# Performance work log

Hardware: AMD Instinct MI355X
Metric: run time of the kernel (lower is better)

The kernel has to match this reference:

```python
import jax, jax.numpy as jnp
import numpy as np

B, L, C = 16, 450, 768
MID = 256
K = 8912
TEMP = 0.07
ENT_TEMP = 0.01
EPS_NORM = 1e-12


def _l2norm(v):
    n = jnp.sqrt(jnp.sum(v * v, axis=-1, keepdims=True))
    return v / jnp.maximum(n, EPS_NORM)


def setup_inputs() -> dict:
    key = jax.random.key(0)
    k1, k2, k3, k4 = jax.random.split(key, 4)
    x = jax.random.normal(k1, (B, L, C), dtype=jnp.float32)
    W_down = jax.random.normal(k2, (C, MID), dtype=jnp.float32) * (1.0 / np.sqrt(C))
    b_down = jnp.zeros((MID,), dtype=jnp.float32)
    bound = 1.0 / np.sqrt(MID)
    embedding = jax.random.uniform(k3, (K, MID), dtype=jnp.float32, minval=-bound, maxval=bound)
    return {"x": x, "W_down": W_down, "b_down": b_down, "embedding": embedding}


def reference(x, W_down, b_down, embedding):
    Bx, Lx, Cx = x.shape
    # down projection: [B,L,C] -> [B,L,MID]
    z = jnp.einsum('blc,cm->blm', x, W_down) + b_down
    zf = z.reshape(Bx * Lx, MID)
    zn = _l2norm(zf)                       # [N, MID]
    en = _l2norm(embedding)                # [K, MID]
    # squared euclidean distance on the unit sphere: ||a-b||^2 = 2 - 2 a.b
    d = 2.0 - 2.0 * jnp.einsum('nm,km->nk', zn, en)   # [N, K]
    idx = jnp.argmin(d, axis=1)            # [N]
    # codebook usage (no-grad stats)
    occ = jnp.bincount(idx, length=K)
    code_book_usage = jnp.mean((occ > 0).astype(jnp.float32))
    # soft assignment probs (hard_quant branch)
    logits = -d / TEMP
    probs = jax.nn.softmax(logits, axis=1)
    z_q = en[idx]                          # [N, MID]
    vq_loss = jnp.mean((z_q - jax.lax.stop_gradient(zn)) ** 2)
    commit_loss = jnp.mean((jax.lax.stop_gradient(z_q) - zn) ** 2)
    # straight-through estimator
    z_q_ste = zn + jax.lax.stop_gradient(z_q - zn)
    # entropy loss on affinity = -d at entropy temperature
    fa = -d / ENT_TEMP
    p = jax.nn.softmax(fa, axis=-1)
    lp = jax.nn.log_softmax(fa, axis=-1)
    avg_probs = jnp.mean(p, axis=0)
    avg_entropy = -jnp.sum(avg_probs * jnp.log(avg_probs + 1e-5))
    sample_entropy = -jnp.mean(jnp.sum(p * lp, axis=-1))
    entropy_loss = sample_entropy - avg_entropy
    return (z_q_ste.reshape(Bx, Lx, MID), probs.reshape(Bx, Lx, K),
            code_book_usage, vq_loss, commit_loss, entropy_loss)
```

## Files before the change

### kernel.cpp

```cpp
#include <hip/hip_runtime.h>
#include <stdint.h>

#define N_TOK 7200
#define N_PAD 7232
#define K_CODE 8912
#define K_PAD 8960
#define N_KT 140
#define MID 256
#define C_DIM 768
#define INV_TEMP (1.0f/0.07f)
#define INV_ETEMP 100.0f
#define MARGIN 0.02f
#define CAND_CAP 64
#define EPS_N 1e-12f

typedef __attribute__((ext_vector_type(8))) short short8;
typedef __attribute__((ext_vector_type(4))) float f32x4;

__device__ __forceinline__ unsigned short f2bf(float f) {
    unsigned u = __float_as_uint(f);
    u += 0x7fffu + ((u >> 16) & 1u);
    return (unsigned short)(u >> 16);
}
__device__ __forceinline__ float bf2f(unsigned short h) {
    return __uint_as_float(((unsigned)h) << 16);
}

__global__ void k_init(float* ap_acc, int* used, float* acc4, int* ccnt) {
    int i = blockIdx.x * 256 + threadIdx.x;
    if (i < K_CODE) { ap_acc[i] = 0.f; used[i] = 0; }
    if (i < N_TOK) ccnt[i] = 0;
    if (i < 4) acc4[i] = 0.f;
}

__global__ void k_wsplit(const float* __restrict__ W,
                         unsigned short* __restrict__ wt_h,
                         unsigned short* __restrict__ wt_l) {
    int i = blockIdx.x * 256 + threadIdx.x;
    if (i >= C_DIM * MID) return;
    int c = i / MID, t = i % MID;
    float v = W[i];
    unsigned short h = f2bf(v);
    unsigned short l = f2bf(v - bf2f(h));
    wt_h[t * C_DIM + c] = h;
    wt_l[t * C_DIM + c] = l;
}

__global__ void k_ennorm(const float* __restrict__ emb,
                         float* __restrict__ en,
                         unsigned short* __restrict__ en_h) {
    int n = blockIdx.x, t = threadIdx.x;
    float v = emb[n * MID + t];
    __shared__ float sb[256];
    sb[t] = v * v; __syncthreads();
    for (int s = 128; s > 0; s >>= 1) { if (t < s) sb[t] += sb[t + s]; __syncthreads(); }
    float nn = sqrtf(sb[0]);
    float o = v / fmaxf(nn, EPS_N);
    en[n * MID + t] = o;
    en_h[n * MID + t] = f2bf(o);
}

__global__ __launch_bounds__(256) void k_zgemm(const float* __restrict__ x,
                                               const unsigned short* __restrict__ wt_h,
                                               const unsigned short* __restrict__ wt_l,
                                               float* __restrict__ zbuf) {
    __shared__ unsigned short ls[4 * 64 * 72];
    unsigned short* xh = ls;
    unsigned short* xl = ls + 64 * 72;
    unsigned short* wh = ls + 2 * 64 * 72;
    unsigned short* wl = ls + 3 * 64 * 72;
    int tid = threadIdx.x;
    int m0 = blockIdx.y * 64;
    int t0 = blockIdx.x * 64;
    int lane = tid & 63, wv = tid >> 6;
    int quad = lane >> 4, l15 = lane & 15;
    int mrow0 = (wv >> 1) * 32, ncol0 = (wv & 1) * 32;
    f32x4 acc[2][2] = {};

    for (int ch = 0; ch < 12; ch++) {
        int c0 = ch * 64;
        for (int it = 0; it < 4; it++) {
            int r = it * 16 + (tid >> 4);
            int cq = tid & 15;
            float4 v = make_float4(0.f, 0.f, 0.f, 0.f);
            int gr = m0 + r;
            if (gr < N_TOK) v = ((const float4*)x)[(size_t)gr * (C_DIM / 4) + (c0 >> 2) + cq];
            unsigned short h0 = f2bf(v.x), h1 = f2bf(v.y), h2 = f2bf(v.z), h3 = f2bf(v.w);
            ushort4 hh = make_ushort4(h0, h1, h2, h3);
            ushort4 ll = make_ushort4(f2bf(v.x - bf2f(h0)), f2bf(v.y - bf2f(h1)),
                                      f2bf(v.z - bf2f(h2)), f2bf(v.w - bf2f(h3)));
            *((ushort4*)&xh[r * 72 + cq * 4]) = hh;
            *((ushort4*)&xl[r * 72 + cq * 4]) = ll;
        }
        for (int it = 0; it < 2; it++) {
            int r = it * 32 + (tid >> 3);
            int cq = tid & 7;
            uint4 vh = ((const uint4*)wt_h)[(size_t)(t0 + r) * (C_DIM / 8) + (c0 >> 3) + cq];
            uint4 vl = ((const uint4*)wt_l)[(size_t)(t0 + r) * (C_DIM / 8) + (c0 >> 3) + cq];
            *((uint4*)&wh[r * 72 + cq * 8]) = vh;
            *((uint4*)&wl[r * 72 + cq * 8]) = vl;
        }
        __syncthreads();
        for (int ks = 0; ks < 2; ks++) {
            int co = ks * 32 + quad * 8;
            short8 ah0 = *((const short8*)&xh[(mrow0 + l15) * 72 + co]);
            short8 ah1 = *((const short8*)&xh[(mrow0 + 16 + l15) * 72 + co]);
            short8 al0 = *((const short8*)&xl[(mrow0 + l15) * 72 + co]);
            short8 al1 = *((const short8*)&xl[(mrow0 + 16 + l15) * 72 + co]);
            short8 bh0 = *((const short8*)&wh[(ncol0 + l15) * 72 + co]);
            short8 bh1 = *((const short8*)&wh[(ncol0 + 16 + l15) * 72 + co]);
            short8 bl0 = *((const short8*)&wl[(ncol0 + l15) * 72 + co]);
            short8 bl1 = *((const short8*)&wl[(ncol0 + 16 + l15) * 72 + co]);
            acc[0][0] = __builtin_amdgcn_mfma_f32_16x16x32_bf16(ah0, bh0, acc[0][0], 0, 0, 0);
            acc[0][1] = __builtin_amdgcn_mfma_f32_16x16x32_bf16(ah0, bh1, acc[0][1], 0, 0, 0);
            acc[1][0] = __builtin_amdgcn_mfma_f32_16x16x32_bf16(ah1, bh0, acc[1][0], 0, 0, 0);
            acc[1][1] = __builtin_amdgcn_mfma_f32_16x16x32_bf16(ah1, bh1, acc[1][1], 0, 0, 0);
            acc[0][0] = __builtin_amdgcn_mfma_f32_16x16x32_bf16(ah0, bl0, acc[0][0], 0, 0, 0);
            acc[0][1] = __builtin_amdgcn_mfma_f32_16x16x32_bf16(ah0, bl1, acc[0][1], 0, 0, 0);
            acc[1][0] = __builtin_amdgcn_mfma_f32_16x16x32_bf16(ah1, bl0, acc[1][0], 0, 0, 0);
            acc[1][1] = __builtin_amdgcn_mfma_f32_16x16x32_bf16(ah1, bl1, acc[1][1], 0, 0, 0);
            acc[0][0] = __builtin_amdgcn_mfma_f32_16x16x32_bf16(al0, bh0, acc[0][0], 0, 0, 0);
            acc[0][1] = __builtin_amdgcn_mfma_f32_16x16x32_bf16(al0, bh1, acc[0][1], 0, 0, 0);
            acc[1][0] = __builtin_amdgcn_mfma_f32_16x16x32_bf16(al1, bh0, acc[1][0], 0, 0, 0);
            acc[1][1] = __builtin_amdgcn_mfma_f32_16x16x32_bf16(al1, bh1, acc[1][1], 0, 0, 0);
        }
        __syncthreads();
    }
    for (int i = 0; i < 2; i++)
        for (int j = 0; j < 2; j++)
            for (int r = 0; r < 4; r++) {
                int gr = m0 + mrow0 + i * 16 + quad * 4 + r;
                int gc = t0 + ncol0 + j * 16 + l15;
                if (gr < N_TOK) zbuf[(size_t)gr * MID + gc] = acc[i][j][r];
            }
}

__global__ void k_znorm(float* __restrict__ zbuf, const float* __restrict__ b_down,
                        unsigned short* __restrict__ zn_h) {
    int n = blockIdx.x, t = threadIdx.x;
    float v = zbuf[(size_t)n * MID + t] + b_down[t];
    __shared__ float sb[256];
    sb[t] = v * v; __syncthreads();
    for (int s = 128; s > 0; s >>= 1) { if (t < s) sb[t] += sb[t + s]; __syncthreads(); }
    float nn = sqrtf(sb[0]);
    float o = v / fmaxf(nn, EPS_N);
    zbuf[(size_t)n * MID + t] = o;
    zn_h[(size_t)n * MID + t] = f2bf(o);
}

template<int PASS>
__global__ __launch_bounds__(256) void k_dpass(const unsigned short* __restrict__ zn_h,
                                               const unsigned short* __restrict__ en_h,
                                               float4* __restrict__ part4,
                                               const float* __restrict__ rs_m,
                                               const float* __restrict__ rs_ist,
                                               const float* __restrict__ rs_is1,
                                               float* __restrict__ ap_acc,
                                               float* __restrict__ out1,
                                               int* __restrict__ ccnt,
                                               int* __restrict__ cand) {
    __shared__ __align__(16) char smem[2 * 64 * 136 * 2];
    unsigned short* at = (unsigned short*)smem;
    unsigned short* bt = at + 64 * 136;
    int tid = threadIdx.x;
    int kt = blockIdx.x, mt = blockIdx.y;
    int m0 = mt * 64, k0c = kt * 64;
    int lane = tid & 63, wv = tid >> 6;
    int quad = lane >> 4, l15 = lane & 15;
    int mrow0 = (wv >> 1) * 32, ncol0 = (wv & 1) * 32;
    f32x4 acc[2][2] = {};

    for (int ch = 0; ch < 2; ch++) {
        int c0 = ch * 128;
        for (int it = 0; it < 4; it++) {
            int r = it * 16 + (tid >> 4);
            int cq = tid & 15;
            uint4 va = ((const uint4*)zn_h)[(size_t)(m0 + r) * (MID / 8) + (c0 >> 3) + cq];
            uint4 vb = ((const uint4*)en_h)[(size_t)(k0c + r) * (MID / 8) + (c0 >> 3) + cq];
            *((uint4*)&at[r * 136 + cq * 8]) = va;
            *((uint4*)&bt[r * 136 + cq * 8]) = vb;
        }
        __syncthreads();
        for (int ks = 0; ks < 4; ks++) {
            int co = ks * 32 + quad * 8;
            short8 a0 = *((const short8*)&at[(mrow0 + l15) * 136 + co]);
            short8 a1 = *((const short8*)&at[(mrow0 + 16 + l15) * 136 + co]);
            short8 b0 = *((const short8*)&bt[(ncol0 + l15) * 136 + co]);
            short8 b1 = *((const short8*)&bt[(ncol0 + 16 + l15) * 136 + co]);
            acc[0][0] = __builtin_amdgcn_mfma_f32_16x16x32_bf16(a0, b0, acc[0][0], 0, 0, 0);
            acc[0][1] = __builtin_amdgcn_mfma_f32_16x16x32_bf16(a0, b1, acc[0][1], 0, 0, 0);
            acc[1][0] = __builtin_amdgcn_mfma_f32_16x16x32_bf16(a1, b0, acc[1][0], 0, 0, 0);
            acc[1][1] = __builtin_amdgcn_mfma_f32_16x16x32_bf16(a1, b1, acc[1][1], 0, 0, 0);
        }
        __syncthreads();
    }

    float* sd = (float*)smem;
    float* lm = sd + 64 * 68;
    float* lt = lm + 64;
    float* l1 = lt + 64;
    float* colacc = l1 + 64;

    if (PASS == 2) {
        if (tid < 64) {
            int gr = m0 + tid;
            bool okr = gr < N_TOK;
            lm[tid] = okr ? rs_m[gr] : 0.f;
            lt[tid] = okr ? rs_ist[gr] : 0.f;
            l1[tid] = okr ? rs_is1[gr] : 0.f;
        }
    }
    for (int i = 0; i < 2; i++)
        for (int j = 0; j < 2; j++)
            for (int r = 0; r < 4; r++) {
                int lr = mrow0 + i * 16 + quad * 4 + r;
                int lc = ncol0 + j * 16 + l15;
                int gc = k0c + lc;
                float dv = (gc < K_CODE) ? (2.f - 2.f * acc[i][j][r]) : 1e30f;
                sd[lr * 68 + lc] = dv;
            }
    __syncthreads();

    if (PASS == 1) {
        int rloc = wv * 16 + (lane >> 2);
        const float* rowp = sd + rloc * 68 + (lane & 3) * 16;
        float vals[16];
        float vmin = 1e30f;
        #pragma unroll
        for (int i = 0; i < 16; i++) { vals[i] = rowp[i]; vmin = fminf(vmin, vals[i]); }
        vmin = fminf(vmin, __shfl_xor(vmin, 1));
        vmin = fminf(vmin, __shfl_xor(vmin, 2));
        float st = 0.f, s1 = 0.f, s2 = 0.f;
        #pragma unroll
        for (int i = 0; i < 16; i++) {
            float dd = vmin - vals[i];
            st += __expf(dd * INV_TEMP);
            float te = dd * INV_ETEMP;
            float e = __expf(te);
            s1 += e; s2 += e * te;
        }
        st += __shfl_xor(st, 1); st += __shfl_xor(st, 2);
        s1 += __shfl_xor(s1, 1); s1 += __shfl_xor(s1, 2);
        s2 += __shfl_xor(s2, 1); s2 += __shfl_xor(s2, 2);
        if ((lane & 3) == 0) {
            int gr = m0 + rloc;
            if (gr < N_TOK) part4[(size_t)gr * N_KT + kt] = make_float4(vmin, st, s1, s2);
        }
    } else {
        int col = tid & 63, rq = tid >> 6;
        float ce = 0.f;
        #pragma unroll
        for (int r16 = 0; r16 < 16; r16++) {
            int lr = rq * 16 + r16;
            float dv = sd[lr * 68 + col];
            ce += __expf((lm[lr] - dv) * INV_ETEMP) * l1[lr];
        }
        colacc[rq * 64 + col] = ce;
        __syncthreads();
        if (tid < 64) {
            float s = colacc[tid] + colacc[64 + tid] + colacc[128 + tid] + colacc[192 + tid];
            int gc = k0c + tid;
            if (gc < K_CODE) atomicAdd(&ap_acc[gc], s);
        }
        #pragma unroll
        for (int it = 0; it < 4; it++) {
            int idx = it * 256 + tid;
            int lr = idx >> 4, c4 = idx & 15;
            int gr = m0 + lr;
            if (gr >= N_TOK) continue;
            int gc = k0c + c4 * 4;
            if (gc >= K_CODE) continue;
            float4 v = *((const float4*)(sd + lr * 68 + c4 * 4));
            float mm = lm[lr], tt = lt[lr];
            float thr = mm + MARGIN;
            if (v.x <= thr) { int p = atomicAdd(&ccnt[gr], 1); if (p < CAND_CAP) cand[gr * CAND_CAP + p] = gc + 0; }
            if (v.y <= thr) { int p = atomicAdd(&ccnt[gr], 1); if (p < CAND_CAP) cand[gr * CAND_CAP + p] = gc + 1; }
            if (v.z <= thr) { int p = atomicAdd(&ccnt[gr], 1); if (p < CAND_CAP) cand[gr * CAND_CAP + p] = gc + 2; }
            if (v.w <= thr) { int p = atomicAdd(&ccnt[gr], 1); if (p < CAND_CAP) cand[gr * CAND_CAP + p] = gc + 3; }
            float4 p;
            p.x = __expf((mm - v.x) * INV_TEMP) * tt;
            p.y = __expf((mm - v.y) * INV_TEMP) * tt;
            p.z = __expf((mm - v.z) * INV_TEMP) * tt;
            p.w = __expf((mm - v.w) * INV_TEMP) * tt;
            *((float4*)(out1 + (size_t)gr * K_CODE + gc)) = p;
        }
    }
}

__global__ void k_combine(const float4* __restrict__ part4,
                          float* __restrict__ rs_m, float* __restrict__ rs_ist,
                          float* __restrict__ rs_is1,
                          float* __restrict__ acc4) {
    int sub = threadIdx.x >> 6;
    int row = blockIdx.x * 4 + sub;
    int l = threadIdx.x & 63;
    float4 pv[3];
    float m = 1e30f;
    #pragma unroll
    for (int c = 0; c < 3; c++) {
        int t = l + c * 64;
        pv[c] = (t < N_KT) ? part4[(size_t)row * N_KT + t] : make_float4(1e30f, 0.f, 0.f, 0.f);
        m = fminf(m, pv[c].x);
    }
    #pragma unroll
    for (int s = 1; s < 64; s <<= 1) m = fminf(m, __shfl_xor(m, s));
    float st = 0.f, s1 = 0.f, s2 = 0.f;
    #pragma unroll
    for (int c = 0; c < 3; c++) {
        float mb = pv[c].x;
        int t = l + c * 64;
        if (t < N_KT && mb < 1e29f) {
            float dT = (m - mb) * INV_TEMP;
            st += __expf(dT) * pv[c].y;
            float dE = (m - mb) * INV_ETEMP;
            float e = __expf(dE);
            s1 += e * pv[c].z;
            s2 += e * (pv[c].w + dE * pv[c].z);
        }
    }
    #pragma unroll
    for (int s = 1; s < 64; s <<= 1) {
        st += __shfl_xor(st, s);
        s1 += __shfl_xor(s1, s);
        s2 += __shfl_xor(s2, s);
    }
    if (l == 0) {
        rs_m[row] = m;
        rs_ist[row] = 1.f / st;
        rs_is1[row] = 1.f / s1;
        atomicAdd(&acc4[1], s2 / s1 - __logf(s1));
    }
}

__global__ void k_refine(const float* __restrict__ zn, const float* __restrict__ en,
                         const int* __restrict__ ccnt, const int* __restrict__ cand,
                         int* __restrict__ idxb, int* __restrict__ used,
                         float* __restrict__ acc4) {
    int n = blockIdx.x * 4 + (threadIdx.x >> 6);
    int lane = threadIdx.x & 63;
    if (n >= N_TOK) return;
    int cnt = ccnt[n];
    if (cnt > CAND_CAP) cnt = CAND_CAP;
    float4 a = ((const float4*)(zn + (size_t)n * MID))[lane];
    float best = 1e30f; int bj = K_CODE;
    for (int c = 0; c < cnt; c++) {
        int code = cand[n * CAND_CAP + c];
        float4 b = ((const float4*)(en + (size_t)code * MID))[lane];
        float s = a.x * b.x + a.y * b.y + a.z * b.z + a.w * b.w;
        #pragma unroll
        for (int off = 1; off < 64; off <<= 1) s += __shfl_xor(s, off);
        float dist = 2.f - 2.f * s;
        if (dist < best || (dist == best && code < bj)) { best = dist; bj = code; }
    }
    float4 b = ((const float4*)(en + (size_t)bj * MID))[lane];
    float dx = b.x - a.x, dy = b.y - a.y, dz = b.z - a.z, dw = b.w - a.w;
    float sq = dx * dx + dy * dy + dz * dz + dw * dw;
    #pragma unroll
    for (int off = 32; off > 0; off >>= 1) sq += __shfl_down(sq, off);
    if (lane == 0) {
        idxb[n] = bj;
        used[bj] = 1;
        atomicAdd(&acc4[0], sq);
    }
}

__global__ void k_out0(const float* __restrict__ en, const int* __restrict__ idxb,
                       float* __restrict__ out0) {
    int n = blockIdx.x, t = threadIdx.x;
    int j = idxb[n];
    out0[(size_t)n * MID + t] = en[(size_t)j * MID + t];
}

__global__ void k_scal(const int* __restrict__ used, const float* __restrict__ ap_acc,
                       const float* __restrict__ acc4, float* __restrict__ outs) {
    int t = threadIdx.x;
    float uSum = 0.f, aeSum = 0.f;
    for (int k = t; k < K_CODE; k += 256) {
        uSum += (float)used[k];
        float ap = ap_acc[k] * (1.0f / (float)N_TOK);
        aeSum += ap * __logf(ap + 1e-5f);
    }
    __shared__ float sb[256];
    sb[t] = uSum; __syncthreads();
    for (int s = 128; s > 0; s >>= 1) { if (t < s) sb[t] += sb[t + s]; __syncthreads(); }
    uSum = sb[0];
    __syncthreads(); sb[t] = aeSum; __syncthreads();
    for (int s = 128; s > 0; s >>= 1) { if (t < s) sb[t] += sb[t + s]; __syncthreads(); }
    aeSum = sb[0];
    if (t == 0) {
        outs[0] = uSum / (float)K_CODE;
        float vq = acc4[0] / (float)((size_t)N_TOK * MID);
        outs[1] = vq;
        outs[2] = vq;
        outs[3] = -(acc4[1] / (float)N_TOK) + aeSum;
    }
}

extern "C" void kernel_launch(void* const* d_in, const int* in_sizes, int n_in,
                              void* d_out, int out_size, void* d_ws, size_t ws_size,
                              hipStream_t stream) {
    const float* x   = (const float*)d_in[0];
    const float* W   = (const float*)d_in[1];
    const float* b   = (const float*)d_in[2];
    const float* emb = (const float*)d_in[3];

    float* out  = (float*)d_out;
    float* out0 = out;
    float* out1 = out + (size_t)N_TOK * MID;
    float* outs = out + (size_t)N_TOK * MID + (size_t)N_TOK * K_CODE;

    char* w = (char*)d_ws;
    size_t off = 0;
    auto carve = [&](size_t bytes) { void* p = w + off; off += (bytes + 255) & ~(size_t)255; return p; };
    float*          zn    = (float*)         carve((size_t)N_PAD * MID * 4);
    float*          en    = (float*)         carve((size_t)K_PAD * MID * 4);
    unsigned short* zn_h  = (unsigned short*)carve((size_t)N_PAD * MID * 2);
    unsigned short* en_h  = (unsigned short*)carve((size_t)K_PAD * MID * 2);
    unsigned short* wt_h  = (unsigned short*)carve((size_t)MID * C_DIM * 2);
    unsigned short* wt_l  = (unsigned short*)carve((size_t)MID * C_DIM * 2);
    float4*         part4 = (float4*)        carve((size_t)N_TOK * N_KT * 16);
    float*          rs_m  = (float*)         carve((size_t)N_TOK * 4);
    float*          rs_ist= (float*)         carve((size_t)N_TOK * 4);
    float*          rs_is1= (float*)         carve((size_t)N_TOK * 4);
    int*            ccnt  = (int*)           carve((size_t)N_TOK * 4);
    int*            cand  = (int*)           carve((size_t)N_TOK * CAND_CAP * 4);
    int*            idxb  = (int*)           carve((size_t)N_TOK * 4);
    float*          ap_acc= (float*)         carve((size_t)K_CODE * 4);
    int*            used  = (int*)           carve((size_t)K_CODE * 4);
    float*          acc4  = (float*)         carve(16);
    (void)ws_size; (void)in_sizes; (void)n_in; (void)out_size;

    k_init   <<<35, 256, 0, stream>>>(ap_acc, used, acc4, ccnt);
    k_wsplit <<<(C_DIM * MID + 255) / 256, 256, 0, stream>>>(W, wt_h, wt_l);
    k_ennorm <<<K_CODE, 256, 0, stream>>>(emb, en, en_h);
    k_zgemm  <<<dim3(4, 113), 256, 0, stream>>>(x, wt_h, wt_l, zn);
    k_znorm  <<<N_TOK, 256, 0, stream>>>(zn, b, zn_h);
    k_dpass<1><<<dim3(N_KT, 113), 256, 0, stream>>>(zn_h, en_h, part4, rs_m, rs_ist, rs_is1, ap_acc, out1, ccnt, cand);
    k_combine<<<N_TOK / 4, 256, 0, stream>>>(part4, rs_m, rs_ist, rs_is1, acc4);
    k_dpass<2><<<dim3(N_KT, 113), 256, 0, stream>>>(zn_h, en_h, part4, rs_m, rs_ist, rs_is1, ap_acc, out1, ccnt, cand);
    k_refine <<<N_TOK / 4, 256, 0, stream>>>(zn, en, ccnt, cand, idxb, used, acc4);
    k_out0   <<<N_TOK, 256, 0, stream>>>(en, idxb, out0);
    k_scal   <<<1, 256, 0, stream>>>(used, ap_acc, acc4, outs);
}
```

Before: 670.4 us.

## Use 128x128 tiles with direct global-to-LDS loads in distance passes

Both distance-matrix passes move from 64x64 to 128x128 output tiles, giving each wave a 4x4 MFMA grid and more operand reuse per LDS load. Operand loads use global_load_lds with an XOR-swizzled LDS layout in place of padded register staging. The epilogues now work directly on accumulator registers with cross-lane shuffles, skipping the LDS distance scratch tile. Per-token probability stores become scalar strided writes rather than float4, and the zn_h/en_h padding rows are zeroed in init so the larger tiles read clean data.

```diff
diff --git a/kernel.cpp b/kernel.cpp
--- a/kernel.cpp
+++ b/kernel.cpp
@@ -3,9 +3,12 @@
 
 #define N_TOK 7200
 #define N_PAD 7232
+#define N_PAD_A 7296
 #define K_CODE 8912
 #define K_PAD 8960
 #define N_KT 140
+#define NKT128 70
+#define NMT128 57
 #define MID 256
 #define C_DIM 768
 #define INV_TEMP (1.0f/0.07f)
@@ -26,11 +29,21 @@
     return __uint_as_float(((unsigned)h) << 16);
 }
 
-__global__ void k_init(float* ap_acc, int* used, float* acc4, int* ccnt) {
+__device__ __forceinline__ void gload16(const void* g, void* l) {
+    __builtin_amdgcn_global_load_lds(
+        (const __attribute__((address_space(1))) unsigned int*)g,
+        (__attribute__((address_space(3))) unsigned int*)l,
+        16, 0, 0);
+}
+
+__global__ void k_init(float* ap_acc, int* used, float* acc4, int* ccnt,
+                       unsigned short* zn_h, unsigned short* en_h) {
     int i = blockIdx.x * 256 + threadIdx.x;
     if (i < K_CODE) { ap_acc[i] = 0.f; used[i] = 0; }
     if (i < N_TOK) ccnt[i] = 0;
     if (i < 4) acc4[i] = 0.f;
+    for (int j = i; j < (N_PAD_A - N_TOK) * MID; j += 8960) zn_h[(size_t)N_TOK * MID + j] = 0;
+    for (int j = i; j < (K_PAD - K_CODE) * MID; j += 8960) en_h[(size_t)K_CODE * MID + j] = 0;
 }
 
 __global__ void k_wsplit(const float* __restrict__ W,
@@ -159,130 +172,145 @@
                                                float* __restrict__ out1,
                                                int* __restrict__ ccnt,
                                                int* __restrict__ cand) {
-    __shared__ __align__(16) char smem[2 * 64 * 136 * 2];
-    unsigned short* at = (unsigned short*)smem;
-    unsigned short* bt = at + 64 * 136;
+    __shared__ __align__(16) unsigned short lds[2 * 128 * 64];
+    unsigned short* lA = lds;
+    unsigned short* lB = lds + 128 * 64;
     int tid = threadIdx.x;
     int kt = blockIdx.x, mt = blockIdx.y;
-    int m0 = mt * 64, k0c = kt * 64;
+    int m0 = mt * 128, k0 = kt * 128;
     int lane = tid & 63, wv = tid >> 6;
     int quad = lane >> 4, l15 = lane & 15;
-    int mrow0 = (wv >> 1) * 32, ncol0 = (wv & 1) * 32;
-    f32x4 acc[2][2] = {};
-
-    for (int ch = 0; ch < 2; ch++) {
-        int c0 = ch * 128;
+    int wr = wv >> 1, wc = wv & 1;
+    f32x4 acc[4][4] = {};
+
+    int sr = tid >> 3;
+    int scb = (tid & 7) * 16;
+
+    for (int step = 0; step < 4; step++) {
+        int cB = step * 128;
+        #pragma unroll
         for (int it = 0; it < 4; it++) {
-            int r = it * 16 + (tid >> 4);
-            int cq = tid & 15;
-            uint4 va = ((const uint4*)zn_h)[(size_t)(m0 + r) * (MID / 8) + (c0 >> 3) + cq];
-            uint4 vb = ((const uint4*)en_h)[(size_t)(k0c + r) * (MID / 8) + (c0 >> 3) + cq];
-            *((uint4*)&at[r * 136 + cq * 8]) = va;
-            *((uint4*)&bt[r * 136 + cq * 8]) = vb;
-        }
-        __syncthreads();
-        for (int ks = 0; ks < 4; ks++) {
-            int co = ks * 32 + quad * 8;
-            short8 a0 = *((const short8*)&at[(mrow0 + l15) * 136 + co]);
-            short8 a1 = *((const short8*)&at[(mrow0 + 16 + l15) * 136 + co]);
-            short8 b0 = *((const short8*)&bt[(ncol0 + l15) * 136 + co]);
-            short8 b1 = *((const short8*)&bt[(ncol0 + 16 + l15) * 136 + co]);
-            acc[0][0] = __builtin_amdgcn_mfma_f32_16x16x32_bf16(a0, b0, acc[0][0], 0, 0, 0);
-            acc[0][1] = __builtin_amdgcn_mfma_f32_16x16x32_bf16(a0, b1, acc[0][1], 0, 0, 0);
-            acc[1][0] = __builtin_amdgcn_mfma_f32_16x16x32_bf16(a1, b0, acc[1][0], 0, 0, 0);
-            acc[1][1] = __builtin_amdgcn_mfma_f32_16x16x32_bf16(a1, b1, acc[1][1], 0, 0, 0);
-        }
-        __syncthreads();
-    }
-
-    float* sd = (float*)smem;
-    float* lm = sd + 64 * 68;
-    float* lt = lm + 64;
-    float* l1 = lt + 64;
-    float* colacc = l1 + 64;
-
-    if (PASS == 2) {
-        if (tid < 64) {
+            int r = it * 32 + sr;
+            int srcb = scb ^ ((r & 7) << 4);
+            const char* gA = (const char*)zn_h + (size_t)(m0 + r) * 512 + cB + srcb;
+            const char* gB = (const char*)en_h + (size_t)(k0 + r) * 512 + cB + srcb;
+            gload16(gA, (char*)lA + it * 4096 + wv * 1024);
+            gload16(gB, (char*)lB + it * 4096 + wv * 1024);
+        }
+        __syncthreads();
+        #pragma unroll
+        for (int ks = 0; ks < 2; ks++) {
+            short8 a[4], b[4];
+            #pragma unroll
+            for (int i = 0; i < 4; i++) {
+                int ra = wr * 64 + i * 16 + l15;
+                int ca = (ks * 64 + quad * 16) ^ ((ra & 7) << 4);
+                a[i] = *(const short8*)((const char*)lA + ra * 128 + ca);
+                int rb = wc * 64 + i * 16 + l15;
+                int cb2 = (ks * 64 + quad * 16) ^ ((rb & 7) << 4);
+                b[i] = *(const short8*)((const char*)lB + rb * 128 + cb2);
+            }
+            #pragma unroll
+            for (int i = 0; i < 4; i++)
+                #pragma unroll
+                for (int j = 0; j < 4; j++)
+                    acc[i][j] = __builtin_amdgcn_mfma_f32_16x16x32_bf16(a[i], b[j], acc[i][j], 0, 0, 0);
+        }
+        __syncthreads();
+    }
+
+    if (PASS == 1) {
+        int kth = kt * 2 + wc;
+        #pragma unroll
+        for (int i = 0; i < 4; i++) {
+            #pragma unroll
+            for (int r = 0; r < 4; r++) {
+                float dv[4]; float vmin = 1e30f;
+                #pragma unroll
+                for (int j = 0; j < 4; j++) {
+                    int gc = k0 + wc * 64 + j * 16 + l15;
+                    float d = 2.f - 2.f * acc[i][j][r];
+                    dv[j] = (gc < K_CODE) ? d : 1e30f;
+                    vmin = fminf(vmin, dv[j]);
+                }
+                vmin = fminf(vmin, __shfl_xor(vmin, 1));
+                vmin = fminf(vmin, __shfl_xor(vmin, 2));
+                vmin = fminf(vmin, __shfl_xor(vmin, 4));
+                vmin = fminf(vmin, __shfl_xor(vmin, 8));
+                float st = 0.f, s1 = 0.f, s2 = 0.f;
+                #pragma unroll
+                for (int j = 0; j < 4; j++) {
+                    float dd = vmin - dv[j];
+                    st += __expf(dd * INV_TEMP);
+                    float te = dd * INV_ETEMP;
+                    float e = __expf(te);
+                    s1 += e; s2 += e * te;
+                }
+                st += __shfl_xor(st, 1); st += __shfl_xor(st, 2);
+                st += __shfl_xor(st, 4); st += __shfl_xor(st, 8);
+                s1 += __shfl_xor(s1, 1); s1 += __shfl_xor(s1, 2);
+                s1 += __shfl_xor(s1, 4); s1 += __shfl_xor(s1, 8);
+                s2 += __shfl_xor(s2, 1); s2 += __shfl_xor(s2, 2);
+                s2 += __shfl_xor(s2, 4); s2 += __shfl_xor(s2, 8);
+                if (l15 == 0) {
+                    int gr = m0 + wr * 64 + i * 16 + quad * 4 + r;
+                    if (gr < N_TOK) part4[(size_t)gr * N_KT + kth] = make_float4(vmin, st, s1, s2);
+                }
+            }
+        }
+    } else {
+        float* lm = (float*)lds;
+        float* lt_ = lm + 128;
+        float* l1_ = lt_ + 128;
+        float* colacc = l1_ + 128;
+        if (tid < 128) {
             int gr = m0 + tid;
-            bool okr = gr < N_TOK;
-            lm[tid] = okr ? rs_m[gr] : 0.f;
-            lt[tid] = okr ? rs_ist[gr] : 0.f;
-            l1[tid] = okr ? rs_is1[gr] : 0.f;
-        }
-    }
-    for (int i = 0; i < 2; i++)
-        for (int j = 0; j < 2; j++)
+            bool ok = gr < N_TOK;
+            lm[tid]  = ok ? rs_m[gr]   : 0.f;
+            lt_[tid] = ok ? rs_ist[gr] : 0.f;
+            l1_[tid] = ok ? rs_is1[gr] : 0.f;
+        }
+        __syncthreads();
+        float ce[4] = {0.f, 0.f, 0.f, 0.f};
+        #pragma unroll
+        for (int i = 0; i < 4; i++) {
+            #pragma unroll
             for (int r = 0; r < 4; r++) {
-                int lr = mrow0 + i * 16 + quad * 4 + r;
-                int lc = ncol0 + j * 16 + l15;
-                int gc = k0c + lc;
-                float dv = (gc < K_CODE) ? (2.f - 2.f * acc[i][j][r]) : 1e30f;
-                sd[lr * 68 + lc] = dv;
+                int lr = wr * 64 + i * 16 + quad * 4 + r;
+                int gr = m0 + lr;
+                float m_ = lm[lr], t_ = lt_[lr], i1 = l1_[lr];
+                bool okr = gr < N_TOK;
+                float thr = m_ + MARGIN;
+                #pragma unroll
+                for (int j = 0; j < 4; j++) {
+                    int gc = k0 + wc * 64 + j * 16 + l15;
+                    if (okr && gc < K_CODE) {
+                        float d = 2.f - 2.f * acc[i][j][r];
+                        ce[j] += __expf((m_ - d) * INV_ETEMP) * i1;
+                        float p = __expf((m_ - d) * INV_TEMP) * t_;
+                        out1[(size_t)gr * K_CODE + gc] = p;
+                        if (d <= thr) {
+                            int pd = atomicAdd(&ccnt[gr], 1);
+                            if (pd < CAND_CAP) cand[gr * CAND_CAP + pd] = gc;
+                        }
+                    }
+                }
             }
-    __syncthreads();
-
-    if (PASS == 1) {
-        int rloc = wv * 16 + (lane >> 2);
-        const float* rowp = sd + rloc * 68 + (lane & 3) * 16;
-        float vals[16];
-        float vmin = 1e30f;
-        #pragma unroll
-        for (int i = 0; i < 16; i++) { vals[i] = rowp[i]; vmin = fminf(vmin, vals[i]); }
-        vmin = fminf(vmin, __shfl_xor(vmin, 1));
-        vmin = fminf(vmin, __shfl_xor(vmin, 2));
-        float st = 0.f, s1 = 0.f, s2 = 0.f;
-        #pragma unroll
-        for (int i = 0; i < 16; i++) {
-            float dd = vmin - vals[i];
-            st += __expf(dd * INV_TEMP);
-            float te = dd * INV_ETEMP;
-            float e = __expf(te);
-            s1 += e; s2 += e * te;
-        }
-        st += __shfl_xor(st, 1); st += __shfl_xor(st, 2);
-        s1 += __shfl_xor(s1, 1); s1 += __shfl_xor(s1, 2);
-        s2 += __shfl_xor(s2, 1); s2 += __shfl_xor(s2, 2);
-        if ((lane & 3) == 0) {
-            int gr = m0 + rloc;
-            if (gr < N_TOK) part4[(size_t)gr * N_KT + kt] = make_float4(vmin, st, s1, s2);
-        }
-    } else {
-        int col = tid & 63, rq = tid >> 6;
-        float ce = 0.f;
-        #pragma unroll
-        for (int r16 = 0; r16 < 16; r16++) {
-            int lr = rq * 16 + r16;
-            float dv = sd[lr * 68 + col];
-            ce += __expf((lm[lr] - dv) * INV_ETEMP) * l1[lr];
-        }
-        colacc[rq * 64 + col] = ce;
-        __syncthreads();
-        if (tid < 64) {
-            float s = colacc[tid] + colacc[64 + tid] + colacc[128 + tid] + colacc[192 + tid];
-            int gc = k0c + tid;
-            if (gc < K_CODE) atomicAdd(&ap_acc[gc], s);
-        }
-        #pragma unroll
-        for (int it = 0; it < 4; it++) {
-            int idx = it * 256 + tid;
-            int lr = idx >> 4, c4 = idx & 15;
-            int gr = m0 + lr;
-            if (gr >= N_TOK) continue;
-            int gc = k0c + c4 * 4;
-            if (gc >= K_CODE) continue;
-            float4 v = *((const float4*)(sd + lr * 68 + c4 * 4));
-            float mm = lm[lr], tt = lt[lr];
-            float thr = mm + MARGIN;
-            if (v.x <= thr) { int p = atomicAdd(&ccnt[gr], 1); if (p < CAND_CAP) cand[gr * CAND_CAP + p] = gc + 0; }
-            if (v.y <= thr) { int p = atomicAdd(&ccnt[gr], 1); if (p < CAND_CAP) cand[gr * CAND_CAP + p] = gc + 1; }
-            if (v.z <= thr) { int p = atomicAdd(&ccnt[gr], 1); if (p < CAND_CAP) cand[gr * CAND_CAP + p] = gc + 2; }
-            if (v.w <= thr) { int p = atomicAdd(&ccnt[gr], 1); if (p < CAND_CAP) cand[gr * CAND_CAP + p] = gc + 3; }
-            float4 p;
-            p.x = __expf((mm - v.x) * INV_TEMP) * tt;
-            p.y = __expf((mm - v.y) * INV_TEMP) * tt;
-            p.z = __expf((mm - v.z) * INV_TEMP) * tt;
-            p.w = __expf((mm - v.w) * INV_TEMP) * tt;
-            *((float4*)(out1 + (size_t)gr * K_CODE + gc)) = p;
+        }
+        #pragma unroll
+        for (int j = 0; j < 4; j++) {
+            ce[j] += __shfl_xor(ce[j], 16);
+            ce[j] += __shfl_xor(ce[j], 32);
+        }
+        if (quad == 0) {
+            #pragma unroll
+            for (int j = 0; j < 4; j++)
+                colacc[wr * 128 + wc * 64 + j * 16 + l15] = ce[j];
+        }
+        __syncthreads();
+        if (tid < 128) {
+            int gc = k0 + tid;
+            if (gc < K_CODE) atomicAdd(&ap_acc[gc], colacc[tid] + colacc[128 + tid]);
         }
     }
 }
@@ -414,7 +442,7 @@
     auto carve = [&](size_t bytes) { void* p = w + off; off += (bytes + 255) & ~(size_t)255; return p; };
     float*          zn    = (float*)         carve((size_t)N_PAD * MID * 4);
     float*          en    = (float*)         carve((size_t)K_PAD * MID * 4);
-    unsigned short* zn_h  = (unsigned short*)carve((size_t)N_PAD * MID * 2);
+    unsigned short* zn_h  = (unsigned short*)carve((size_t)N_PAD_A * MID * 2);
     unsigned short* en_h  = (unsigned short*)carve((size_t)K_PAD * MID * 2);
     unsigned short* wt_h  = (unsigned short*)carve((size_t)MID * C_DIM * 2);
     unsigned short* wt_l  = (unsigned short*)carve((size_t)MID * C_DIM * 2);
@@ -430,14 +458,14 @@
     float*          acc4  = (float*)         carve(16);
     (void)ws_size; (void)in_sizes; (void)n_in; (void)out_size;
 
-    k_init   <<<35, 256, 0, stream>>>(ap_acc, used, acc4, ccnt);
+    k_init   <<<35, 256, 0, stream>>>(ap_acc, used, acc4, ccnt, zn_h, en_h);
     k_wsplit <<<(C_DIM * MID + 255) / 256, 256, 0, stream>>>(W, wt_h, wt_l);
     k_ennorm <<<K_CODE, 256, 0, stream>>>(emb, en, en_h);
     k_zgemm  <<<dim3(4, 113), 256, 0, stream>>>(x, wt_h, wt_l, zn);
     k_znorm  <<<N_TOK, 256, 0, stream>>>(zn, b, zn_h);
-    k_dpass<1><<<dim3(N_KT, 113), 256, 0, stream>>>(zn_h, en_h, part4, rs_m, rs_ist, rs_is1, ap_acc, out1, ccnt, cand);
+    k_dpass<1><<<dim3(NKT128, NMT128), 256, 0, stream>>>(zn_h, en_h, part4, rs_m, rs_ist, rs_is1, ap_acc, out1, ccnt, cand);
     k_combine<<<N_TOK / 4, 256, 0, stream>>>(part4, rs_m, rs_ist, rs_is1, acc4);
-    k_dpass<2><<<dim3(N_KT, 113), 256, 0, stream>>>(zn_h, en_h, part4, rs_m, rs_ist, rs_is1, ap_acc, out1, ccnt, cand);
+    k_dpass<2><<<dim3(NKT128, NMT128), 256, 0, stream>>>(zn_h, en_h, part4, rs_m, rs_ist, rs_is1, ap_acc, out1, ccnt, cand);
     k_refine <<<N_TOK / 4, 256, 0, stream>>>(zn, en, ccnt, cand, idxb, used, acc4);
     k_out0   <<<N_TOK, 256, 0, stream>>>(en, idxb, out0);
     k_scal   <<<1, 256, 0, stream>>>(used, ap_acc, acc4, outs);
```

New measurement: 682.8 us. Within noise of the previous version (+1.8%).

## Merge prep kernels, pre-split x to bf16 pairs, fold out0 gather into refine

Applied to the files above, without the earlier changes.

The init, weight-split and embedding-normalize kernels are merged into one k_prep launch. That launch also splits x into bf16 hi/lo arrays in global memory, and the z GEMM now reads those arrays instead of converting x on every tile load. The separate k_out0 gather kernel is removed; k_refine writes the chosen codeword to out0 itself. This cuts launch count and redundant conversion work, since each x tile was converted once per column block (4 times). In exchange it adds an extra global round trip of about 22 MB for the split x arrays.

```diff
diff --git a/kernel.cpp b/kernel.cpp
--- a/kernel.cpp
+++ b/kernel.cpp
@@ -26,41 +26,49 @@
     return __uint_as_float(((unsigned)h) << 16);
 }
 
-__global__ void k_init(float* ap_acc, int* used, float* acc4, int* ccnt) {
-    int i = blockIdx.x * 256 + threadIdx.x;
-    if (i < K_CODE) { ap_acc[i] = 0.f; used[i] = 0; }
-    if (i < N_TOK) ccnt[i] = 0;
-    if (i < 4) acc4[i] = 0.f;
-}
-
-__global__ void k_wsplit(const float* __restrict__ W,
-                         unsigned short* __restrict__ wt_h,
-                         unsigned short* __restrict__ wt_l) {
-    int i = blockIdx.x * 256 + threadIdx.x;
-    if (i >= C_DIM * MID) return;
-    int c = i / MID, t = i % MID;
-    float v = W[i];
-    unsigned short h = f2bf(v);
-    unsigned short l = f2bf(v - bf2f(h));
-    wt_h[t * C_DIM + c] = h;
-    wt_l[t * C_DIM + c] = l;
-}
-
-__global__ void k_ennorm(const float* __restrict__ emb,
-                         float* __restrict__ en,
-                         unsigned short* __restrict__ en_h) {
-    int n = blockIdx.x, t = threadIdx.x;
-    float v = emb[n * MID + t];
+__global__ void k_prep(const float* __restrict__ emb,
+                       float* __restrict__ en, unsigned short* __restrict__ en_h,
+                       const float* __restrict__ W,
+                       unsigned short* __restrict__ wt_h, unsigned short* __restrict__ wt_l,
+                       const float* __restrict__ x,
+                       unsigned short* __restrict__ xh_g, unsigned short* __restrict__ xl_g,
+                       float* __restrict__ ap_acc, int* __restrict__ used,
+                       float* __restrict__ acc4, int* __restrict__ ccnt) {
     __shared__ float sb[256];
-    sb[t] = v * v; __syncthreads();
-    for (int s = 128; s > 0; s >>= 1) { if (t < s) sb[t] += sb[t + s]; __syncthreads(); }
-    float nn = sqrtf(sb[0]);
-    float o = v / fmaxf(nn, EPS_N);
-    en[n * MID + t] = o;
-    en_h[n * MID + t] = f2bf(o);
-}
-
-__global__ __launch_bounds__(256) void k_zgemm(const float* __restrict__ x,
+    int b = blockIdx.x, t = threadIdx.x;
+    if (b < K_CODE) {
+        float v = emb[b * MID + t];
+        sb[t] = v * v; __syncthreads();
+        for (int s = 128; s > 0; s >>= 1) { if (t < s) sb[t] += sb[t + s]; __syncthreads(); }
+        float nn = sqrtf(sb[0]);
+        float o = v / fmaxf(nn, EPS_N);
+        en[b * MID + t] = o;
+        en_h[b * MID + t] = f2bf(o);
+    } else if (b < K_CODE + 768) {
+        int i = (b - K_CODE) * 256 + t;
+        int c = i / MID, tc = i % MID;
+        float v = W[i];
+        unsigned short h = f2bf(v);
+        unsigned short l = f2bf(v - bf2f(h));
+        wt_h[tc * C_DIM + c] = h;
+        wt_l[tc * C_DIM + c] = l;
+    } else if (b < K_CODE + 768 + 5400) {
+        size_t i4 = ((size_t)(b - K_CODE - 768) * 256 + t) * 4;
+        float4 v = *(const float4*)(x + i4);
+        unsigned short h0 = f2bf(v.x), h1 = f2bf(v.y), h2 = f2bf(v.z), h3 = f2bf(v.w);
+        *((ushort4*)(xh_g + i4)) = make_ushort4(h0, h1, h2, h3);
+        *((ushort4*)(xl_g + i4)) = make_ushort4(f2bf(v.x - bf2f(h0)), f2bf(v.y - bf2f(h1)),
+                                                f2bf(v.z - bf2f(h2)), f2bf(v.w - bf2f(h3)));
+    } else {
+        int i = (b - K_CODE - 768 - 5400) * 256 + t;
+        if (i < K_CODE) { ap_acc[i] = 0.f; used[i] = 0; }
+        if (i < N_TOK) ccnt[i] = 0;
+        if (i < 4) acc4[i] = 0.f;
+    }
+}
+
+__global__ __launch_bounds__(256) void k_zgemm(const unsigned short* __restrict__ xh_g,
+                                               const unsigned short* __restrict__ xl_g,
                                                const unsigned short* __restrict__ wt_h,
                                                const unsigned short* __restrict__ wt_l,
                                                float* __restrict__ zbuf) {
@@ -79,18 +87,17 @@
 
     for (int ch = 0; ch < 12; ch++) {
         int c0 = ch * 64;
-        for (int it = 0; it < 4; it++) {
-            int r = it * 16 + (tid >> 4);
-            int cq = tid & 15;
-            float4 v = make_float4(0.f, 0.f, 0.f, 0.f);
+        for (int it = 0; it < 2; it++) {
+            int r = it * 32 + (tid >> 3);
+            int cq = tid & 7;
             int gr = m0 + r;
-            if (gr < N_TOK) v = ((const float4*)x)[(size_t)gr * (C_DIM / 4) + (c0 >> 2) + cq];
-            unsigned short h0 = f2bf(v.x), h1 = f2bf(v.y), h2 = f2bf(v.z), h3 = f2bf(v.w);
-            ushort4 hh = make_ushort4(h0, h1, h2, h3);
-            ushort4 ll = make_ushort4(f2bf(v.x - bf2f(h0)), f2bf(v.y - bf2f(h1)),
-                                      f2bf(v.z - bf2f(h2)), f2bf(v.w - bf2f(h3)));
-            *((ushort4*)&xh[r * 72 + cq * 4]) = hh;
-            *((ushort4*)&xl[r * 72 + cq * 4]) = ll;
+            uint4 vh = make_uint4(0, 0, 0, 0), vl = make_uint4(0, 0, 0, 0);
+            if (gr < N_TOK) {
+                vh = ((const uint4*)xh_g)[(size_t)gr * (C_DIM / 8) + (c0 >> 3) + cq];
+                vl = ((const uint4*)xl_g)[(size_t)gr * (C_DIM / 8) + (c0 >> 3) + cq];
+            }
+            *((uint4*)&xh[r * 72 + cq * 8]) = vh;
+            *((uint4*)&xl[r * 72 + cq * 8]) = vl;
         }
         for (int it = 0; it < 2; it++) {
             int r = it * 32 + (tid >> 3);
@@ -335,7 +342,7 @@
 __global__ void k_refine(const float* __restrict__ zn, const float* __restrict__ en,
                          const int* __restrict__ ccnt, const int* __restrict__ cand,
                          int* __restrict__ idxb, int* __restrict__ used,
-                         float* __restrict__ acc4) {
+                         float* __restrict__ acc4, float* __restrict__ out0) {
     int n = blockIdx.x * 4 + (threadIdx.x >> 6);
     int lane = threadIdx.x & 63;
     if (n >= N_TOK) return;
@@ -353,6 +360,7 @@
         if (dist < best || (dist == best && code < bj)) { best = dist; bj = code; }
     }
     float4 b = ((const float4*)(en + (size_t)bj * MID))[lane];
+    ((float4*)(out0 + (size_t)n * MID))[lane] = b;
     float dx = b.x - a.x, dy = b.y - a.y, dz = b.z - a.z, dw = b.w - a.w;
     float sq = dx * dx + dy * dy + dz * dz + dw * dw;
     #pragma unroll
@@ -362,13 +370,6 @@
         used[bj] = 1;
         atomicAdd(&acc4[0], sq);
     }
-}
-
-__global__ void k_out0(const float* __restrict__ en, const int* __restrict__ idxb,
-                       float* __restrict__ out0) {
-    int n = blockIdx.x, t = threadIdx.x;
-    int j = idxb[n];
-    out0[(size_t)n * MID + t] = en[(size_t)j * MID + t];
 }
 
 __global__ void k_scal(const int* __restrict__ used, const float* __restrict__ ap_acc,
@@ -418,6 +419,8 @@
     unsigned short* en_h  = (unsigned short*)carve((size_t)K_PAD * MID * 2);
     unsigned short* wt_h  = (unsigned short*)carve((size_t)MID * C_DIM * 2);
     unsigned short* wt_l  = (unsigned short*)carve((size_t)MID * C_DIM * 2);
+    unsigned short* xh_g  = (unsigned short*)carve((size_t)N_TOK * C_DIM * 2);
+    unsigned short* xl_g  = (unsigned short*)carve((size_t)N_TOK * C_DIM * 2);
     float4*         part4 = (float4*)        carve((size_t)N_TOK * N_KT * 16);
     float*          rs_m  = (float*)         carve((size_t)N_TOK * 4);
     float*          rs_ist= (float*)         carve((size_t)N_TOK * 4);
@@ -430,15 +433,14 @@
     float*          acc4  = (float*)         carve(16);
     (void)ws_size; (void)in_sizes; (void)n_in; (void)out_size;
 
-    k_init   <<<35, 256, 0, stream>>>(ap_acc, used, acc4, ccnt);
-    k_wsplit <<<(C_DIM * MID + 255) / 256, 256, 0, stream>>>(W, wt_h, wt_l);
-    k_ennorm <<<K_CODE, 256, 0, stream>>>(emb, en, en_h);
-    k_zgemm  <<<dim3(4, 113), 256, 0, stream>>>(x, wt_h, wt_l, zn);
+    k_prep   <<<K_CODE + 768 + 5400 + 35, 256, 0, stream>>>(emb, en, en_h, W, wt_h, wt_l,
+                                                            x, xh_g, xl_g,
+                                                            ap_acc, used, acc4, ccnt);
+    k_zgemm  <<<dim3(4, 113), 256, 0, stream>>>(xh_g, xl_g, wt_h, wt_l, zn);
     k_znorm  <<<N_TOK, 256, 0, stream>>>(zn, b, zn_h);
     k_dpass<1><<<dim3(N_KT, 113), 256, 0, stream>>>(zn_h, en_h, part4, rs_m, rs_ist, rs_is1, ap_acc, out1, ccnt, cand);
     k_combine<<<N_TOK / 4, 256, 0, stream>>>(part4, rs_m, rs_ist, rs_is1, acc4);
     k_dpass<2><<<dim3(N_KT, 113), 256, 0, stream>>>(zn_h, en_h, part4, rs_m, rs_ist, rs_is1, ap_acc, out1, ccnt, cand);
-    k_refine <<<N_TOK / 4, 256, 0, stream>>>(zn, en, ccnt, cand, idxb, used, acc4);
-    k_out0   <<<N_TOK, 256, 0, stream>>>(en, idxb, out0);
+    k_refine <<<N_TOK / 4, 256, 0, stream>>>(zn, en, ccnt, cand, idxb, used, acc4, out0);
     k_scal   <<<1, 256, 0, stream>>>(used, ap_acc, acc4, outs);
 }
```

New measurement: 644.1 us. 3.9% less time.
